# Optimization experiments

Measured on AMD Instinct MI355X. Metric: run time of the kernel, lower is better.

The kernel has to match this reference:

```python
import jax, jax.numpy as jnp
import numpy as np

# Module constants (match init_kwargs)
M = 2049                      # NpointsMesh (odd)
TAU = 2.821e-5                # Gaussian spreading width ~ 12*(pi/M)^2
XLIMS = (0.0, 10.0)
L = abs(XLIMS[1] - XLIMS[0])
KGRID = jnp.asarray(np.linspace(-(M // 2), M // 2, M), dtype=jnp.float32)        # (M,)
XGRID = jnp.asarray(2.0 * np.pi * np.linspace(XLIMS[0], XLIMS[1], M + 1)[:-1] / L,
                    dtype=jnp.float32)                                           # (M,)
FOUR_PI = 4.0 * np.pi


def setup_inputs() -> dict:
    key = jax.random.key(0)
    kx, = jax.random.split(key, 1)
    x = jax.random.uniform(kx, (16, 1024), dtype=jnp.float32) * 10.0  # points in [xLims[0], xLims[1])
    ones = jnp.ones((1,), dtype=jnp.float32)  # tf.initializers.ones for all 4 weights
    return {"x": x, "shift0": ones, "amp0": ones, "shift1": ones, "amp1": ones}


def reference(x, shift0, amp0, shift1, amp1):
    # Gaussian spreading: (B, N, M)
    diff = x[..., None] * (2.0 * np.pi / L) - XGRID
    g = jnp.exp(-jnp.square(diff) / (4.0 * TAU))
    # Sum over points -> gridded density (B, M), then FFT + shift
    gsum = jnp.sum(g, axis=1).astype(jnp.complex64)
    fft_g = jnp.fft.fftshift(jnp.fft.fft(gsum, axis=-1), axes=-1) * (L / (2.0 * np.pi))
    # Deconvolution of the Gaussian kernel (real-valued)
    deconv = jnp.sqrt(np.pi / TAU) * jnp.exp(jnp.square(KGRID) * TAU)  # (M,)
    rfft = fft_g * deconv  # (B, M) complex
    # Fourier multipliers (real; imag parts are structurally zero in the original)
    m1 = -amp0 * FOUR_PI / (jnp.square(KGRID) + jnp.square(5.0 * shift0))            # (M,)
    m2 = amp1 * FOUR_PI * jnp.square(1.0 / (jnp.square(KGRID) + jnp.square(5.0 * shift1)))  # (M,)
    mult = jnp.stack([m1, m2], axis=0)  # (2, M)
    mult_fft = mult[None, :, :].astype(jnp.complex64) * rfft[:, None, :]  # (B, 2, M)
    mult_deconv = mult_fft * deconv  # second deconv application, as in the original
    # Inverse FFT back to the mesh, keep real part: (B, 2, M)
    irfft = jnp.real(jnp.fft.ifft(jnp.fft.ifftshift(mult_deconv, axes=-1), axis=-1))
    # Inverse interpolation back to the points: (B, N, 2, M) -> (B, N, 2)
    local = irfft[:, None, :, :] * g[:, :, None, :]
    fmm = jnp.sum(local, axis=-1) / M
    return fmm
```

## Files before the change

kernel.cpp:

```cpp
#include <hip/hip_runtime.h>
#include <math.h>

#define M_   2049
#define B_   16
#define N_   1024
#define TAU_ 2.821e-5
#define PI_  3.14159265358979323846
#define TWO_PI_ 6.283185307179586476925286766559

#define GS_CH    8
#define H_JSPLIT 16
#define CV_SPLIT 16
#define FMM_LPP  16
#define MPAD     2052

#define SW(i) ((i) + ((i) >> 2))

__global__ void spread_h_kernel(const float* __restrict__ x,
                                const float* __restrict__ s0, const float* __restrict__ a0,
                                const float* __restrict__ s1, const float* __restrict__ a1,
                                double* __restrict__ gsum, double* __restrict__ hhalf) {
    __shared__ double smem[M_ + 128];
    const int bx = blockIdx.x;

    if (bx < GS_CH * B_) {
        const int b  = bx / GS_CH;
        const int ch = bx % GS_CH;
        for (int i = threadIdx.x; i < M_; i += 256) smem[i] = 0.0;
        __syncthreads();
        const int pl  = threadIdx.x >> 1;
        const int sub = threadIdx.x & 1;
        const double du      = TWO_PI_ / (double)M_;
        const double inv4tau = 1.0 / (4.0 * TAU_);
        const double u = (double)x[b * N_ + ch * (N_ / GS_CH) + pl] * (TWO_PI_ / 10.0);
        const int mc = (int)(u / du + 0.5);
        const int start = mc - 33 + sub * 34;
        for (int i = 0; i < 34; ++i) {
            int m = start + i;
            if (m >= 0 && m < M_) {
                double d = u - du * (double)m;
                double t = d * d * inv4tau;
                if (t < 88.0) atomicAdd(&smem[m], (double)__expf(-(float)t));
            }
        }
        __syncthreads();
        for (int i = threadIdx.x; i < M_; i += 256) {
            double v = smem[i];
            if (v != 0.0) atomicAdd(&gsum[b * M_ + i], v);
        }
    } else {
        const int t  = bx - GS_CH * B_;
        const int dt = t % 5;
        const int jc = t / 5;
        double* costab = smem;
        double* cf0    = smem + M_;
        double* cf1    = smem + M_ + 64;
        const int jlo = 1 + jc * (1024 / H_JSPLIT);
        const double ang0 = TWO_PI_ / (double)M_;

        for (int i = threadIdx.x; i <= 1024; i += 256) {
            double v = cos(ang0 * (double)i);
            costab[i] = v;
            if (i > 0) costab[M_ - i] = v;
        }
        if (threadIdx.x < 1024 / H_JSPLIT) {
            int j = jlo + threadIdx.x;
            double k2   = (double)j * (double)j;
            double dec2 = (PI_ / TAU_) * exp(2.0 * TAU_ * k2);
            double base = 2.0 * (10.0 / TWO_PI_) * dec2 / (double)M_;
            double sA = 5.0 * (double)s0[0];
            cf0[threadIdx.x] = base * (-(double)a0[0] * 4.0 * PI_ / (k2 + sA * sA));
            double sB = 5.0 * (double)s1[0];
            double den = k2 + sB * sB;
            cf1[threadIdx.x] = base * ((double)a1[0] * 4.0 * PI_ / (den * den));
        }
        __syncthreads();

        const int d = dt * 256 + threadIdx.x;
        if (d > 1024) return;

        double acc0 = 0.0, acc1 = 0.0;
        if (jc == 0) {
            double w0base = (10.0 / TWO_PI_) * (PI_ / TAU_) / (double)M_;
            double sA = 5.0 * (double)s0[0];
            acc0 = w0base * (-(double)a0[0] * 4.0 * PI_ / (sA * sA));
            double sB = 5.0 * (double)s1[0];
            acc1 = w0base * ((double)a1[0] * 4.0 * PI_ / ((sB * sB) * (sB * sB)));
        }
        int r = (int)(((long long)jlo * (long long)d) % M_);
        #pragma unroll 4
        for (int jj = 0; jj < 1024 / H_JSPLIT; ++jj) {
            double cv_ = costab[r];
            acc0 += cf0[jj] * cv_;
            acc1 += cf1[jj] * cv_;
            r += d; if (r >= M_) r -= M_;
        }
        atomicAdd(&hhalf[d], acc0);
        atomicAdd(&hhalf[1025 + d], acc1);
    }
}

__global__ void conv_kernel(const double* __restrict__ gsum, const double* __restrict__ hhalf,
                            double* __restrict__ part) {
    __shared__ double w0s[1456];
    __shared__ double w1s[1456];
    __shared__ double red[512];
    const int mt = blockIdx.x;
    const int s  = blockIdx.y;
    const int b  = blockIdx.z;
    const int m0  = mt * 1024;
    const int p0  = (s * M_) / CV_SPLIT;
    const int p1  = ((s + 1) * M_) / CV_SPLIT;
    const int len = p1 - p0;
    const int wcount = 1024 + len;
    int base = m0 - (p0 + len - 1);
    while (base < 0) base += M_;
    for (int i = threadIdx.x; i < wcount; i += 256) {
        int idx = base + i;
        while (idx >= M_) idx -= M_;
        int d = (idx > 1024) ? (M_ - idx) : idx;
        w0s[SW(i)] = hhalf[d];
        w1s[SW(i)] = hhalf[1025 + d];
    }
    __syncthreads();

    const double* gs = gsum + (size_t)b * M_ + p0;

    int q = 4 * threadIdx.x + len - 1;
    double c0w0 = w0s[SW(q)],   c0w1 = w0s[SW(q+1)], c0w2 = w0s[SW(q+2)], c0w3 = w0s[SW(q+3)];
    double c1w0 = w1s[SW(q)],   c1w1 = w1s[SW(q+1)], c1w2 = w1s[SW(q+2)], c1w3 = w1s[SW(q+3)];
    double a00 = 0.0, a01 = 0.0, a02 = 0.0, a03 = 0.0;
    double a10 = 0.0, a11 = 0.0, a12 = 0.0, a13 = 0.0;
    #pragma unroll 4
    for (int t = 0; t < len; ++t) {
        double g = gs[t];
        a00 += g * c0w0; a01 += g * c0w1; a02 += g * c0w2; a03 += g * c0w3;
        a10 += g * c1w0; a11 += g * c1w1; a12 += g * c1w2; a13 += g * c1w3;
        c0w3 = c0w2; c0w2 = c0w1; c0w1 = c0w0;
        c1w3 = c1w2; c1w2 = c1w1; c1w1 = c1w0;
        --q;
        c0w0 = w0s[SW(q)]; c1w0 = w1s[SW(q)];
    }
    {
        double* pv = part + (((size_t)s * B_ + b) * 2) * MPAD + m0 + 4 * threadIdx.x;
        pv[0]        = a00; pv[1]        = a01; pv[2]        = a02; pv[3]        = a03;
        pv[MPAD + 0] = a10; pv[MPAD + 1] = a11; pv[MPAD + 2] = a12; pv[MPAD + 3] = a13;
    }

    if (mt == 1) {
        double t0 = 0.0, t1 = 0.0;
        if (threadIdx.x < len) {
            double g = gs[threadIdx.x];
            int qq = 1023 + len - threadIdx.x;
            t0 = g * w0s[SW(qq)];
            t1 = g * w1s[SW(qq)];
        }
        red[threadIdx.x]       = t0;
        red[256 + threadIdx.x] = t1;
        __syncthreads();
        for (int off = 128; off > 0; off >>= 1) {
            if (threadIdx.x < off) {
                red[threadIdx.x]       += red[threadIdx.x + off];
                red[256 + threadIdx.x] += red[256 + threadIdx.x + off];
            }
            __syncthreads();
        }
        if (threadIdx.x == 0) {
            double* pv = part + (((size_t)s * B_ + b) * 2) * MPAD;
            pv[2048]        = red[0];
            pv[MPAD + 2048] = red[256];
        }
    }
}

__global__ void reduce_kernel(const double* __restrict__ part, double* __restrict__ conv) {
    const int idx = blockIdx.x * 256 + threadIdx.x;
    if (idx >= B_ * 2 * M_) return;
    const int b  = idx / (2 * M_);
    const int rm = idx - b * 2 * M_;
    const int c  = rm / M_;
    const int m  = rm - c * M_;
    const size_t off = ((size_t)b * 2 + c) * MPAD + m;
    const size_t sstride = (size_t)B_ * 2 * MPAD;
    double acc = 0.0;
    #pragma unroll
    for (int k = 0; k < CV_SPLIT; ++k)
        acc += part[(size_t)k * sstride + off];
    conv[idx] = acc;
}

__global__ void fmm_kernel(const float* __restrict__ x, const double* __restrict__ conv,
                           float* __restrict__ out) {
    const int gid = blockIdx.x * 256 + threadIdx.x;
    const int pt  = gid / FMM_LPP;
    const int sub = gid % FMM_LPP;
    const int b   = pt >> 10;
    const double du      = TWO_PI_ / (double)M_;
    const double inv4tau = 1.0 / (4.0 * TAU_);
    const double u = (double)x[pt] * (TWO_PI_ / 10.0);
    int mc = (int)(u / du + 0.5);
    int lo = mc - 34; if (lo < 0) lo = 0;
    int hi = mc + 34; if (hi > M_ - 1) hi = M_ - 1;
    const double* c0 = conv + (size_t)(b * 2) * M_;
    const double* c1 = c0 + M_;
    double a0 = 0.0, a1 = 0.0;
    for (int m = lo + sub; m <= hi; m += FMM_LPP) {
        double d = u - du * (double)m;
        double g = (double)__expf(-(float)(d * d * inv4tau));
        a0 += g * c0[m];
        a1 += g * c1[m];
    }
    a0 += __shfl_xor(a0, 1); a1 += __shfl_xor(a1, 1);
    a0 += __shfl_xor(a0, 2); a1 += __shfl_xor(a1, 2);
    a0 += __shfl_xor(a0, 4); a1 += __shfl_xor(a1, 4);
    a0 += __shfl_xor(a0, 8); a1 += __shfl_xor(a1, 8);
    if (sub == 0) {
        out[pt * 2 + 0] = (float)(a0 / (double)M_);
        out[pt * 2 + 1] = (float)(a1 / (double)M_);
    }
}

extern "C" void kernel_launch(void* const* d_in, const int* in_sizes, int n_in,
                              void* d_out, int out_size, void* d_ws, size_t ws_size,
                              hipStream_t stream) {
    (void)in_sizes; (void)n_in; (void)out_size; (void)ws_size;
    const float* x  = (const float*)d_in[0];
    const float* s0 = (const float*)d_in[1];
    const float* a0 = (const float*)d_in[2];
    const float* s1 = (const float*)d_in[3];
    const float* a1 = (const float*)d_in[4];
    float* out = (float*)d_out;

    double* gsum  = (double*)d_ws;
    double* hhalf = gsum + B_ * M_;
    double* conv  = hhalf + 2 * 1025;
    double* part  = conv + B_ * 2 * M_;

    hipMemsetAsync(d_ws, 0, (size_t)(B_ * M_ + 2 * 1025) * sizeof(double), stream);

    hipLaunchKernelGGL(spread_h_kernel, dim3(GS_CH * B_ + 5 * H_JSPLIT), dim3(256), 0,
                       stream, x, s0, a0, s1, a1, gsum, hhalf);
    hipLaunchKernelGGL(conv_kernel, dim3(2, CV_SPLIT, B_), dim3(256), 0, stream,
                       gsum, hhalf, part);
    hipLaunchKernelGGL(reduce_kernel, dim3((B_ * 2 * M_ + 255) / 256), dim3(256), 0, stream,
                       part, conv);
    hipLaunchKernelGGL(fmm_kernel, dim3(B_ * N_ * FMM_LPP / 256), dim3(256), 0, stream,
                       x, conv, out);
}
```

Baseline: 91.83 us.

## Drop memset and reduce kernel, fuse reduce into FMM, restructure spreading blocks

The memset is removed by having one block per batch do spreading entirely in shared memory and write gsum directly. The h-table computation now uses 17 blocks that reduce in shared memory instead of using global atomics. The partial-sum reduce is fused into the FMM gather kernel, which stages conv in LDS with one block per batch. The conv kernel caches gsum in LDS and manually unrolls the register rotation. Together these cut kernel launches and global atomics, but launch far fewer blocks (16 for spreading and 16 for FMM), so parallelism drops sharply and each thread loops serially over 68 or 69 mesh points.

```diff
diff --git a/kernel.cpp b/kernel.cpp
--- a/kernel.cpp
+++ b/kernel.cpp
@@ -8,95 +8,100 @@
 #define PI_  3.14159265358979323846
 #define TWO_PI_ 6.283185307179586476925286766559
 
-#define GS_CH    8
-#define H_JSPLIT 16
 #define CV_SPLIT 16
-#define FMM_LPP  16
 #define MPAD     2052
 
+#define K1_SCAT  16
+#define K1_HT    17
+
 #define SW(i) ((i) + ((i) >> 2))
 
-__global__ void spread_h_kernel(const float* __restrict__ x,
-                                const float* __restrict__ s0, const float* __restrict__ a0,
-                                const float* __restrict__ s1, const float* __restrict__ a1,
-                                double* __restrict__ gsum, double* __restrict__ hhalf) {
-    __shared__ double smem[M_ + 128];
-    const int bx = blockIdx.x;
-
-    if (bx < GS_CH * B_) {
-        const int b  = bx / GS_CH;
-        const int ch = bx % GS_CH;
-        for (int i = threadIdx.x; i < M_; i += 256) smem[i] = 0.0;
-        __syncthreads();
-        const int pl  = threadIdx.x >> 1;
-        const int sub = threadIdx.x & 1;
+__global__ __launch_bounds__(256)
+void spread_h2(const float* __restrict__ x,
+               const float* __restrict__ s0, const float* __restrict__ a0,
+               const float* __restrict__ s1, const float* __restrict__ a1,
+               double* __restrict__ gsum, double* __restrict__ hhalf) {
+    __shared__ double smem[4609];
+    const int bx  = blockIdx.x;
+    const int tid = threadIdx.x;
+
+    if (bx < K1_SCAT) {
+        const int b = bx;
+        for (int i = tid; i < M_; i += 256) smem[i] = 0.0;
+        __syncthreads();
         const double du      = TWO_PI_ / (double)M_;
         const double inv4tau = 1.0 / (4.0 * TAU_);
-        const double u = (double)x[b * N_ + ch * (N_ / GS_CH) + pl] * (TWO_PI_ / 10.0);
-        const int mc = (int)(u / du + 0.5);
-        const int start = mc - 33 + sub * 34;
-        for (int i = 0; i < 34; ++i) {
-            int m = start + i;
-            if (m >= 0 && m < M_) {
-                double d = u - du * (double)m;
-                double t = d * d * inv4tau;
-                if (t < 88.0) atomicAdd(&smem[m], (double)__expf(-(float)t));
-            }
-        }
-        __syncthreads();
-        for (int i = threadIdx.x; i < M_; i += 256) {
-            double v = smem[i];
-            if (v != 0.0) atomicAdd(&gsum[b * M_ + i], v);
-        }
+        for (int c = 0; c < 4; ++c) {
+            const int p = (c << 8) + tid;
+            const double xv = (double)x[(b << 10) + p];
+            const double u  = xv * (TWO_PI_ / 10.0);
+            const int mc = (int)(xv * ((double)M_ / 10.0) + 0.5);
+            const int start = mc - 33;
+            for (int i = 0; i < 68; ++i) {
+                int m = start + i;
+                if (m >= 0 && m < M_) {
+                    double d = u - du * (double)m;
+                    double t = d * d * inv4tau;
+                    if (t < 88.0) atomicAdd(&smem[m], (double)__expf(-(float)t));
+                }
+            }
+        }
+        __syncthreads();
+        for (int i = tid; i < M_; i += 256) gsum[b * M_ + i] = smem[i];
     } else {
-        const int t  = bx - GS_CH * B_;
-        const int dt = t % 5;
-        const int jc = t / 5;
+        const int dtile = bx - K1_SCAT;
         double* costab = smem;
-        double* cf0    = smem + M_;
-        double* cf1    = smem + M_ + 64;
-        const int jlo = 1 + jc * (1024 / H_JSPLIT);
+        double* cf0    = smem + 2049;
+        double* cf1    = smem + 3073;
+        double* red    = smem + 4097;
         const double ang0 = TWO_PI_ / (double)M_;
-
-        for (int i = threadIdx.x; i <= 1024; i += 256) {
+        for (int i = tid; i <= 1024; i += 256) {
             double v = cos(ang0 * (double)i);
             costab[i] = v;
             if (i > 0) costab[M_ - i] = v;
         }
-        if (threadIdx.x < 1024 / H_JSPLIT) {
-            int j = jlo + threadIdx.x;
-            double k2   = (double)j * (double)j;
+        const double sA = 5.0 * (double)s0[0], sB = 5.0 * (double)s1[0];
+        const double amp0 = (double)a0[0],     amp1 = (double)a1[0];
+        for (int jj = tid; jj < 1024; jj += 256) {
+            double j  = (double)(jj + 1);
+            double k2 = j * j;
             double dec2 = (PI_ / TAU_) * exp(2.0 * TAU_ * k2);
             double base = 2.0 * (10.0 / TWO_PI_) * dec2 / (double)M_;
-            double sA = 5.0 * (double)s0[0];
-            cf0[threadIdx.x] = base * (-(double)a0[0] * 4.0 * PI_ / (k2 + sA * sA));
-            double sB = 5.0 * (double)s1[0];
+            cf0[jj] = base * (-amp0 * 4.0 * PI_ / (k2 + sA * sA));
             double den = k2 + sB * sB;
-            cf1[threadIdx.x] = base * ((double)a1[0] * 4.0 * PI_ / (den * den));
-        }
-        __syncthreads();
-
-        const int d = dt * 256 + threadIdx.x;
-        if (d > 1024) return;
-
+            cf1[jj] = base * (amp1 * 4.0 * PI_ / (den * den));
+        }
+        __syncthreads();
+        const int dl = tid & 63;
+        const int jq = tid >> 6;
+        const int d  = (dtile << 6) + dl;
         double acc0 = 0.0, acc1 = 0.0;
-        if (jc == 0) {
-            double w0base = (10.0 / TWO_PI_) * (PI_ / TAU_) / (double)M_;
-            double sA = 5.0 * (double)s0[0];
-            acc0 = w0base * (-(double)a0[0] * 4.0 * PI_ / (sA * sA));
-            double sB = 5.0 * (double)s1[0];
-            acc1 = w0base * ((double)a1[0] * 4.0 * PI_ / ((sB * sB) * (sB * sB)));
-        }
-        int r = (int)(((long long)jlo * (long long)d) % M_);
-        #pragma unroll 4
-        for (int jj = 0; jj < 1024 / H_JSPLIT; ++jj) {
-            double cv_ = costab[r];
-            acc0 += cf0[jj] * cv_;
-            acc1 += cf1[jj] * cv_;
-            r += d; if (r >= M_) r -= M_;
-        }
-        atomicAdd(&hhalf[d], acc0);
-        atomicAdd(&hhalf[1025 + d], acc1);
+        if (d <= 1024) {
+            const int jlo = (jq << 8) + 1;
+            int r = (int)(((long long)jlo * (long long)d) % M_);
+            #pragma unroll 4
+            for (int jj = 0; jj < 256; ++jj) {
+                double cv_ = costab[r];
+                acc0 += cf0[(jq << 8) + jj] * cv_;
+                acc1 += cf1[(jq << 8) + jj] * cv_;
+                r += d; if (r >= M_) r -= M_;
+            }
+        }
+        red[(jq << 6) + dl]       = acc0;
+        red[256 + (jq << 6) + dl] = acc1;
+        __syncthreads();
+        if (tid < 64) {
+            const int dd = (dtile << 6) + tid;
+            if (dd <= 1024) {
+                const double w0base = (10.0 / TWO_PI_) * (PI_ / TAU_) / (double)M_;
+                double h0 = w0base * (-amp0 * 4.0 * PI_ / (sA * sA))
+                          + red[tid] + red[64 + tid] + red[128 + tid] + red[192 + tid];
+                double h1 = w0base * (amp1 * 4.0 * PI_ / ((sB * sB) * (sB * sB)))
+                          + red[256 + tid] + red[320 + tid] + red[384 + tid] + red[448 + tid];
+                hhalf[dd]        = h0;
+                hhalf[1025 + dd] = h1;
+            }
+        }
     }
 }
 
@@ -105,6 +110,7 @@
     __shared__ double w0s[1456];
     __shared__ double w1s[1456];
     __shared__ double red[512];
+    __shared__ double gls[132];
     const int mt = blockIdx.x;
     const int s  = blockIdx.y;
     const int b  = blockIdx.z;
@@ -118,39 +124,53 @@
     for (int i = threadIdx.x; i < wcount; i += 256) {
         int idx = base + i;
         while (idx >= M_) idx -= M_;
-        int d = (idx > 1024) ? (M_ - idx) : idx;
-        w0s[SW(i)] = hhalf[d];
-        w1s[SW(i)] = hhalf[1025 + d];
-    }
+        int dd = (idx > 1024) ? (M_ - idx) : idx;
+        w0s[SW(i)] = hhalf[dd];
+        w1s[SW(i)] = hhalf[1025 + dd];
+    }
+    for (int i = threadIdx.x; i < len; i += 256)
+        gls[i] = gsum[(size_t)b * M_ + p0 + i];
     __syncthreads();
 
-    const double* gs = gsum + (size_t)b * M_ + p0;
-
-    int q = 4 * threadIdx.x + len - 1;
-    double c0w0 = w0s[SW(q)],   c0w1 = w0s[SW(q+1)], c0w2 = w0s[SW(q+2)], c0w3 = w0s[SW(q+3)];
-    double c1w0 = w1s[SW(q)],   c1w1 = w1s[SW(q+1)], c1w2 = w1s[SW(q+2)], c1w3 = w1s[SW(q+3)];
-    double a00 = 0.0, a01 = 0.0, a02 = 0.0, a03 = 0.0;
-    double a10 = 0.0, a11 = 0.0, a12 = 0.0, a13 = 0.0;
-    #pragma unroll 4
-    for (int t = 0; t < len; ++t) {
-        double g = gs[t];
-        a00 += g * c0w0; a01 += g * c0w1; a02 += g * c0w2; a03 += g * c0w3;
-        a10 += g * c1w0; a11 += g * c1w1; a12 += g * c1w2; a13 += g * c1w3;
-        c0w3 = c0w2; c0w2 = c0w1; c0w1 = c0w0;
-        c1w3 = c1w2; c1w2 = c1w1; c1w1 = c1w0;
-        --q;
-        c0w0 = w0s[SW(q)]; c1w0 = w1s[SW(q)];
+    const int q = 4 * threadIdx.x + len - 1;
+    double A0 = w0s[SW(q)], A1 = w0s[SW(q+1)], A2 = w0s[SW(q+2)], A3 = w0s[SW(q+3)];
+    double C0 = w1s[SW(q)], C1 = w1s[SW(q+1)], C2 = w1s[SW(q+2)], C3 = w1s[SW(q+3)];
+    double a00=0.0,a01=0.0,a02=0.0,a03=0.0, a10=0.0,a11=0.0,a12=0.0,a13=0.0;
+    int j = q, tt = 0;
+    for (; tt + 4 <= len; tt += 4) {
+        double g;
+        g = gls[tt];
+        a00 += g*A0; a01 += g*A1; a02 += g*A2; a03 += g*A3;
+        a10 += g*C0; a11 += g*C1; a12 += g*C2; a13 += g*C3;
+        A3 = w0s[SW(j-1)]; C3 = w1s[SW(j-1)];
+        g = gls[tt+1];
+        a00 += g*A3; a01 += g*A0; a02 += g*A1; a03 += g*A2;
+        a10 += g*C3; a11 += g*C0; a12 += g*C1; a13 += g*C2;
+        A2 = w0s[SW(j-2)]; C2 = w1s[SW(j-2)];
+        g = gls[tt+2];
+        a00 += g*A2; a01 += g*A3; a02 += g*A0; a03 += g*A1;
+        a10 += g*C2; a11 += g*C3; a12 += g*C0; a13 += g*C1;
+        A1 = w0s[SW(j-3)]; C1 = w1s[SW(j-3)];
+        g = gls[tt+3];
+        a00 += g*A1; a01 += g*A2; a02 += g*A3; a03 += g*A0;
+        a10 += g*C1; a11 += g*C2; a12 += g*C3; a13 += g*C0;
+        A0 = w0s[SW(j-4)]; C0 = w1s[SW(j-4)];
+        j -= 4;
+    }
+    for (; tt < len; ++tt) {
+        double g = gls[tt];
+        a00 += g*A0; a01 += g*A1; a02 += g*A2; a03 += g*A3;
+        a10 += g*C0; a11 += g*C1; a12 += g*C2; a13 += g*C3;
     }
     {
         double* pv = part + (((size_t)s * B_ + b) * 2) * MPAD + m0 + 4 * threadIdx.x;
         pv[0]        = a00; pv[1]        = a01; pv[2]        = a02; pv[3]        = a03;
         pv[MPAD + 0] = a10; pv[MPAD + 1] = a11; pv[MPAD + 2] = a12; pv[MPAD + 3] = a13;
     }
-
     if (mt == 1) {
         double t0 = 0.0, t1 = 0.0;
         if (threadIdx.x < len) {
-            double g = gs[threadIdx.x];
+            double g = gls[threadIdx.x];
             int qq = 1023 + len - threadIdx.x;
             t0 = g * w0s[SW(qq)];
             t1 = g * w1s[SW(qq)];
@@ -173,50 +193,42 @@
     }
 }
 
-__global__ void reduce_kernel(const double* __restrict__ part, double* __restrict__ conv) {
-    const int idx = blockIdx.x * 256 + threadIdx.x;
-    if (idx >= B_ * 2 * M_) return;
-    const int b  = idx / (2 * M_);
-    const int rm = idx - b * 2 * M_;
-    const int c  = rm / M_;
-    const int m  = rm - c * M_;
-    const size_t off = ((size_t)b * 2 + c) * MPAD + m;
+__global__ __launch_bounds__(256)
+void reduce_fmm(const float* __restrict__ x, const double* __restrict__ part,
+                float* __restrict__ out) {
+    __shared__ double convs[2 * M_];
+    const int b   = blockIdx.x;
+    const int tid = threadIdx.x;
     const size_t sstride = (size_t)B_ * 2 * MPAD;
-    double acc = 0.0;
-    #pragma unroll
-    for (int k = 0; k < CV_SPLIT; ++k)
-        acc += part[(size_t)k * sstride + off];
-    conv[idx] = acc;
-}
-
-__global__ void fmm_kernel(const float* __restrict__ x, const double* __restrict__ conv,
-                           float* __restrict__ out) {
-    const int gid = blockIdx.x * 256 + threadIdx.x;
-    const int pt  = gid / FMM_LPP;
-    const int sub = gid % FMM_LPP;
-    const int b   = pt >> 10;
+    for (int ch = 0; ch < 2; ++ch) {
+        const size_t off0 = ((size_t)b * 2 + ch) * MPAD;
+        for (int m = tid; m < M_; m += 256) {
+            double acc = 0.0;
+            #pragma unroll
+            for (int k = 0; k < CV_SPLIT; ++k)
+                acc += part[(size_t)k * sstride + off0 + m];
+            convs[ch * M_ + m] = acc;
+        }
+    }
+    __syncthreads();
     const double du      = TWO_PI_ / (double)M_;
     const double inv4tau = 1.0 / (4.0 * TAU_);
-    const double u = (double)x[pt] * (TWO_PI_ / 10.0);
-    int mc = (int)(u / du + 0.5);
-    int lo = mc - 34; if (lo < 0) lo = 0;
-    int hi = mc + 34; if (hi > M_ - 1) hi = M_ - 1;
-    const double* c0 = conv + (size_t)(b * 2) * M_;
-    const double* c1 = c0 + M_;
-    double a0 = 0.0, a1 = 0.0;
-    for (int m = lo + sub; m <= hi; m += FMM_LPP) {
-        double d = u - du * (double)m;
-        double g = (double)__expf(-(float)(d * d * inv4tau));
-        a0 += g * c0[m];
-        a1 += g * c1[m];
-    }
-    a0 += __shfl_xor(a0, 1); a1 += __shfl_xor(a1, 1);
-    a0 += __shfl_xor(a0, 2); a1 += __shfl_xor(a1, 2);
-    a0 += __shfl_xor(a0, 4); a1 += __shfl_xor(a1, 4);
-    a0 += __shfl_xor(a0, 8); a1 += __shfl_xor(a1, 8);
-    if (sub == 0) {
-        out[pt * 2 + 0] = (float)(a0 / (double)M_);
-        out[pt * 2 + 1] = (float)(a1 / (double)M_);
+    for (int c = 0; c < 4; ++c) {
+        const int p  = (b << 10) + (c << 8) + tid;
+        const double xv = (double)x[p];
+        const double u  = xv * (TWO_PI_ / 10.0);
+        int mc = (int)(xv * ((double)M_ / 10.0) + 0.5);
+        int lo = mc - 34; if (lo < 0) lo = 0;
+        int hi = mc + 34; if (hi > M_ - 1) hi = M_ - 1;
+        double av0 = 0.0, av1 = 0.0;
+        for (int m = lo; m <= hi; ++m) {
+            double d = u - du * (double)m;
+            double g = (double)__expf(-(float)(d * d * inv4tau));
+            av0 += g * convs[m];
+            av1 += g * convs[M_ + m];
+        }
+        out[p * 2 + 0] = (float)(av0 / (double)M_);
+        out[p * 2 + 1] = (float)(av1 / (double)M_);
     }
 }
 
@@ -233,17 +245,12 @@
 
     double* gsum  = (double*)d_ws;
     double* hhalf = gsum + B_ * M_;
-    double* conv  = hhalf + 2 * 1025;
-    double* part  = conv + B_ * 2 * M_;
-
-    hipMemsetAsync(d_ws, 0, (size_t)(B_ * M_ + 2 * 1025) * sizeof(double), stream);
-
-    hipLaunchKernelGGL(spread_h_kernel, dim3(GS_CH * B_ + 5 * H_JSPLIT), dim3(256), 0,
-                       stream, x, s0, a0, s1, a1, gsum, hhalf);
+    double* part  = hhalf + 2 * 1025;
+
+    hipLaunchKernelGGL(spread_h2, dim3(K1_SCAT + K1_HT), dim3(256), 0, stream,
+                       x, s0, a0, s1, a1, gsum, hhalf);
     hipLaunchKernelGGL(conv_kernel, dim3(2, CV_SPLIT, B_), dim3(256), 0, stream,
                        gsum, hhalf, part);
-    hipLaunchKernelGGL(reduce_kernel, dim3((B_ * 2 * M_ + 255) / 256), dim3(256), 0, stream,
-                       part, conv);
-    hipLaunchKernelGGL(fmm_kernel, dim3(B_ * N_ * FMM_LPP / 256), dim3(256), 0, stream,
-                       x, conv, out);
-}
+    hipLaunchKernelGGL(reduce_fmm, dim3(B_), dim3(256), 0, stream,
+                       x, part, out);
+}
```

Result: slower. 117.1 us (+27.5%).
